# Kernel optimization log

Hardware: AMD Instinct MI355X
Metric: run time of the kernel (lower is better)

The kernel has to match this reference:

```python
import jax, jax.numpy as jnp
import numpy as np
from jax import lax

N_NODES = 100000
N_EDGES = 1600000
NUM_GRAPHS = 2000
F_IN = 64
HIDDEN = 64
NUM_LAYERS = 3
K = 7
NUM_CLASSES = 10


def setup_inputs() -> dict:
    key = jax.random.key(0)
    ks = jax.random.split(key, 16)
    x = jax.random.normal(ks[0], (N_NODES, F_IN), jnp.float32)
    edge_index = jax.random.randint(ks[1], (2, N_EDGES), 0, N_NODES)
    batch = jnp.sort(jax.random.randint(ks[2], (N_NODES,), 0, NUM_GRAPHS))
    s = 1.0 / np.sqrt(HIDDEN)
    p = lambda k_, sh: jax.random.uniform(k_, sh, jnp.float32, -s, s)
    return dict(
        x=x, edge_index=edge_index, batch=batch,
        W1l=p(ks[3], (F_IN, HIDDEN)), b1=p(ks[4], (HIDDEN,)), W1r=p(ks[5], (F_IN, HIDDEN)),
        W2l=p(ks[6], (HIDDEN, HIDDEN)), b2=p(ks[7], (HIDDEN,)), W2r=p(ks[8], (HIDDEN, HIDDEN)),
        W3l=p(ks[9], (HIDDEN, HIDDEN)), b3=p(ks[10], (HIDDEN,)), W3r=p(ks[11], (HIDDEN, HIDDEN)),
        conv1d_w=p(ks[12], (32, HIDDEN, NUM_LAYERS)), conv1d_b=jnp.zeros((32,), jnp.float32),
        lin1_w=p(ks[13], (32 * (K - NUM_LAYERS + 1), HIDDEN)), lin1_b=jnp.zeros((HIDDEN,), jnp.float32),
        lin2_w=p(ks[14], (HIDDEN, NUM_CLASSES)), lin2_b=jnp.zeros((NUM_CLASSES,), jnp.float32),
    )


def _sage(x, src, dst, Wl, b, Wr):
    # PyG SAGEConv (aggr='mean'): lin_l(mean_j x_j) + lin_r(x_i); lin_l carries the bias.
    n = x.shape[0]
    msum = jax.ops.segment_sum(x[src], dst, num_segments=n)          # [N, D] gather+scatter
    cnt = jax.ops.segment_sum(jnp.ones((src.shape[0],), x.dtype), dst, num_segments=n)
    mean = msum / jnp.maximum(cnt, 1.0)[:, None]
    return mean @ Wl + b + x @ Wr


def _sort_pool(x, batch, num_graphs, k):
    # SortAggregation: per graph, sort nodes descending by last feature channel,
    # keep top-k, zero-pad short graphs, flatten to [B, k*D].
    N, D = x.shape
    perm = jnp.lexsort((-x[:, -1], batch))  # primary: graph id, secondary: desc last channel
    sb = batch[perm]
    counts = jax.ops.segment_sum(jnp.ones((N,), jnp.int32), batch, num_segments=num_graphs)
    starts = jnp.concatenate([jnp.zeros((1,), jnp.int32), jnp.cumsum(counts)[:-1]])
    rank = jnp.arange(N, dtype=jnp.int32) - starts[sb]
    valid = rank < k
    b_idx = jnp.where(valid, sb, num_graphs)  # route overflow nodes to dummy row
    r_idx = jnp.where(valid, rank, 0)
    out = jnp.zeros((num_graphs + 1, k, D), x.dtype).at[b_idx, r_idx].set(x[perm])
    return out[:num_graphs].reshape(num_graphs, k * D)


def reference(x, edge_index, batch, W1l, b1, W1r, W2l, b2, W2r, W3l, b3, W3r,
              conv1d_w, conv1d_b, lin1_w, lin1_b, lin2_w, lin2_b):
    src, dst = edge_index[0], edge_index[1]
    h = jax.nn.relu(_sage(x, src, dst, W1l, b1, W1r))
    h = jax.nn.relu(_sage(h, src, dst, W2l, b2, W2r))
    h = jax.nn.relu(_sage(h, src, dst, W3l, b3, W3r))
    g = _sort_pool(h, batch, NUM_GRAPHS, K)                       # [B, K*H]
    g = g.reshape(NUM_GRAPHS, K, HIDDEN).transpose(0, 2, 1)       # [B, H, K]
    c = lax.conv_general_dilated(g, conv1d_w, (1,), 'VALID',
                                 dimension_numbers=('NCH', 'OIH', 'NCH'))
    c = jax.nn.relu(c + conv1d_b[None, :, None])                  # [B, 32, K-ks+1]
    flat = c.reshape(NUM_GRAPHS, -1)
    h1 = jax.nn.relu(flat @ lin1_w + lin1_b)                      # dropout = identity (eval)
    logits = h1 @ lin2_w + lin2_b
    return jax.nn.log_softmax(logits, axis=-1)
```

## Files before the change

### kernel.cpp

```cpp
#include <hip/hip_runtime.h>
#include <hip/hip_bf16.h>

#define NN 100000
#define NE 1600000
#define NG 2000
#define KTOP 7
#define KCAP 192

#define BNODES 128
#define NBKT 782
#define EPB 8192
#define NL1B 196
#define L2CAP 4096

#define GEMM_BLOCKS 768
#define NTILES 1563
#define SMEM_FLOATS (64 * 68 + 2 * 64 * 64)

#define ACC4(A, V) do { A.x += V.x; A.y += V.y; A.z += V.z; A.w += V.w; } while (0)
#define ACC4P(A, U, W) do { A.x += U.x + W.x; A.y += U.y + W.y; \
                            A.z += U.z + W.z; A.w += U.w + W.w; } while (0)

__device__ __forceinline__ void agg_node(const float* __restrict__ XLp, const int* __restrict__ ce,
        int s, int e, int fo, float4& a0, float4& a1, float4& a2, float4& a3) {
    int a = s;
    for (; a + 2 <= e; a += 2) {
        const float4* p0 = (const float4*)(XLp + ((size_t)ce[a] << 6) + fo);
        const float4* p1 = (const float4*)(XLp + ((size_t)ce[a + 1] << 6) + fo);
        float4 u0 = p0[0], u1 = p0[1], u2 = p0[2], u3 = p0[3];
        float4 w0 = p1[0], w1 = p1[1], w2 = p1[2], w3 = p1[3];
        ACC4P(a0, u0, w0); ACC4P(a1, u1, w1); ACC4P(a2, u2, w2); ACC4P(a3, u3, w3);
    }
    if (a < e) {
        const float4* p0 = (const float4*)(XLp + ((size_t)ce[a] << 6) + fo);
        float4 u0 = p0[0], u1 = p0[1], u2 = p0[2], u3 = p0[3];
        ACC4(a0, u0); ACC4(a1, u1); ACC4(a2, u2); ACC4(a3, u3);
    }
}

__device__ __forceinline__ void relu_mean_res(float inv, const float4* tp,
        float4& h0, float4& h1, float4& h2, float4& h3) {
    float4 t0 = tp[0], t1 = tp[1], t2 = tp[2], t3 = tp[3];
    h0.x = fmaxf(h0.x * inv + t0.x, 0.f); h0.y = fmaxf(h0.y * inv + t0.y, 0.f);
    h0.z = fmaxf(h0.z * inv + t0.z, 0.f); h0.w = fmaxf(h0.w * inv + t0.w, 0.f);
    h1.x = fmaxf(h1.x * inv + t1.x, 0.f); h1.y = fmaxf(h1.y * inv + t1.y, 0.f);
    h1.z = fmaxf(h1.z * inv + t1.z, 0.f); h1.w = fmaxf(h1.w * inv + t1.w, 0.f);
    h2.x = fmaxf(h2.x * inv + t2.x, 0.f); h2.y = fmaxf(h2.y * inv + t2.y, 0.f);
    h2.z = fmaxf(h2.z * inv + t2.z, 0.f); h2.w = fmaxf(h2.w * inv + t2.w, 0.f);
    h3.x = fmaxf(h3.x * inv + t3.x, 0.f); h3.y = fmaxf(h3.y * inv + t3.y, 0.f);
    h3.z = fmaxf(h3.z * inv + t3.z, 0.f); h3.w = fmaxf(h3.w * inv + t3.w, 0.f);
}

__device__ __forceinline__ float compute_key(int i, const float* __restrict__ keycol,
        const float* __restrict__ tcol, const int* __restrict__ ptr,
        const int* __restrict__ ce) {
    int s = ptr[i], e = ptr[i + 1];
    float acc = 0.f;
    int a = s;
    for (; a + 2 <= e; a += 2) acc += keycol[ce[a]] + keycol[ce[a + 1]];
    if (a < e) acc += keycol[ce[a]];
    float inv = 1.f / fmaxf((float)(e - s), 1.f);
    return fmaxf(acc * inv + tcol[i], 0.f);
}

#define FMA4C(av, B, acc) do { \
    acc[0] = fmaf(av, B.x, acc[0]); acc[1] = fmaf(av, B.y, acc[1]); \
    acc[2] = fmaf(av, B.z, acc[2]); acc[3] = fmaf(av, B.w, acc[3]); } while (0)

__device__ __forceinline__ void gemm_tile(const float* As, const float* Bl, const float* Br,
        int n0, int ty4, int tx4, float b0, float b1v, float b2v, float b3v,
        float* __restrict__ XL, float* __restrict__ T,
        float* __restrict__ kc_out, float* __restrict__ tc_out) {
    float accl[4][4] = {{0.f}}, accr[4][4] = {{0.f}};
    for (int kc = 0; kc < 64; kc += 4) {
        float4 Av[4], L[4], R[4];
        #pragma unroll
        for (int i = 0; i < 4; ++i) Av[i] = *(const float4*)&As[(ty4 + i) * 68 + kc];
        #pragma unroll
        for (int j = 0; j < 4; ++j) {
            L[j] = *(const float4*)&Bl[(kc + j) * 64 + tx4];
            R[j] = *(const float4*)&Br[(kc + j) * 64 + tx4];
        }
        #pragma unroll
        for (int i = 0; i < 4; ++i) {
            FMA4C(Av[i].x, L[0], accl[i]); FMA4C(Av[i].y, L[1], accl[i]);
            FMA4C(Av[i].z, L[2], accl[i]); FMA4C(Av[i].w, L[3], accl[i]);
            FMA4C(Av[i].x, R[0], accr[i]); FMA4C(Av[i].y, R[1], accr[i]);
            FMA4C(Av[i].z, R[2], accr[i]); FMA4C(Av[i].w, R[3], accr[i]);
        }
    }
    #pragma unroll
    for (int i = 0; i < 4; ++i) {
        int g = n0 + ty4 + i;
        if (g < NN) {
            *(float4*)&XL[(size_t)g * 64 + tx4] =
                make_float4(accl[i][0], accl[i][1], accl[i][2], accl[i][3]);
            *(float4*)&T[(size_t)g * 64 + tx4] =
                make_float4(accr[i][0] + b0, accr[i][1] + b1v, accr[i][2] + b2v, accr[i][3] + b3v);
            if (kc_out && tx4 == 60) {
                kc_out[g] = accl[i][3];
                tc_out[g] = accr[i][3] + b3v;
            }
        }
    }
}

__device__ __forceinline__ void stage_weights(float* Bl, float* Br,
        const float* __restrict__ Wl, const float* __restrict__ Wr, int t) {
    #pragma unroll
    for (int q = 0; q < 4; ++q) {
        int idx = t + q * 256;
        ((float4*)Bl)[idx] = ((const float4*)Wl)[idx];
        ((float4*)Br)[idx] = ((const float4*)Wr)[idx];
    }
}

__device__ __forceinline__ void gemm_body(int bid, int nblocks, float* smem,
        const float* __restrict__ X, const float* __restrict__ Wl,
        const float* __restrict__ Wr, const float* __restrict__ bias,
        float* __restrict__ XL, float* __restrict__ T) {
    float* As = smem;
    float* Bl = smem + 64 * 68;
    float* Br = Bl + 64 * 64;
    int t = threadIdx.x;
    stage_weights(Bl, Br, Wl, Wr, t);
    int ty4 = (t >> 4) * 4, tx4 = (t & 15) * 4;
    float b0 = bias[tx4 + 0], b1v = bias[tx4 + 1], b2v = bias[tx4 + 2], b3v = bias[tx4 + 3];
    for (int tile = bid; tile < NTILES; tile += nblocks) {
        int n0 = tile * 64;
        #pragma unroll
        for (int q = 0; q < 4; ++q) {
            int f = t + q * 256;
            int node = f >> 4, seg = f & 15;
            int g = n0 + node;
            float4 v = make_float4(0.f, 0.f, 0.f, 0.f);
            if (g < NN) v = *(const float4*)&X[(size_t)g * 64 + seg * 4];
            *(float4*)&As[node * 68 + seg * 4] = v;
        }
        __syncthreads();
        gemm_tile(As, Bl, Br, n0, ty4, tx4, b0, b1v, b2v, b3v, XL, T, nullptr, nullptr);
        __syncthreads();
    }
}

__global__ __launch_bounds__(256) void k_aggemm(const float* __restrict__ XL_in,
        float* __restrict__ T, const int* __restrict__ ptr, const int* __restrict__ ce,
        const float* __restrict__ Wl, const float* __restrict__ Wr,
        const float* __restrict__ bias, float* __restrict__ XL_out,
        float* __restrict__ kc_out, float* __restrict__ tc_out) {
    __shared__ float smem[SMEM_FLOATS];
    float* As = smem;
    float* Bl = smem + 64 * 68;
    float* Br = Bl + 64 * 64;
    int t = threadIdx.x;
    stage_weights(Bl, Br, Wl, Wr, t);
    int node_l = t >> 2;
    int fo = (t & 3) * 16;
    int ty4 = (t >> 4) * 4, tx4 = (t & 15) * 4;
    float b0 = bias[tx4 + 0], b1v = bias[tx4 + 1], b2v = bias[tx4 + 2], b3v = bias[tx4 + 3];
    for (int tile = blockIdx.x; tile < NTILES; tile += GEMM_BLOCKS) {
        int n0 = tile * 64;
        int i = n0 + node_l;
        float4 h0 = make_float4(0.f, 0.f, 0.f, 0.f), h1 = h0, h2 = h0, h3 = h0;
        if (i < NN) {
            int s = ptr[i], e = ptr[i + 1];
            agg_node(XL_in, ce, s, e, fo, h0, h1, h2, h3);
            float inv = 1.f / fmaxf((float)(e - s), 1.f);
            relu_mean_res(inv, (const float4*)(T + ((size_t)i << 6) + fo), h0, h1, h2, h3);
        }
        float* dst = &As[node_l * 68 + fo];
        ((float4*)dst)[0] = h0; ((float4*)dst)[1] = h1;
        ((float4*)dst)[2] = h2; ((float4*)dst)[3] = h3;
        __syncthreads();
        gemm_tile(As, Bl, Br, n0, ty4, tx4, b0, b1v, b2v, b3v, XL_out, T, kc_out, tc_out);
        __syncthreads();
    }
}

__global__ __launch_bounds__(256) void k_front(const float* __restrict__ X,
        const float* __restrict__ Wl, const float* __restrict__ Wr,
        const float* __restrict__ bias, float* __restrict__ XL, float* __restrict__ T,
        const int* __restrict__ edst, int* __restrict__ bh_t,
        const int* __restrict__ bat, int* __restrict__ gstart) {
    __shared__ float smem[SMEM_FLOATS];
    int bid = blockIdx.x, t = threadIdx.x;
    if (bid < GEMM_BLOCKS) {
        gemm_body(bid, GEMM_BLOCKS, smem, X, Wl, Wr, bias, XL, T);
    } else if (bid < GEMM_BLOCKS + NL1B) {
        int bk = bid - GEMM_BLOCKS;
        int* h = (int*)smem;
        for (int q = t; q < NBKT; q += 256) h[q] = 0;
        __syncthreads();
        int e0 = bk * EPB, e1 = min(e0 + EPB, NE);
        for (int e = e0 + t; e < e1; e += 256) atomicAdd(&h[edst[e] >> 7], 1);
        __syncthreads();
        for (int q = t; q < NBKT; q += 256) bh_t[q * NL1B + bk] = h[q];
    } else {
        int g = (bid - GEMM_BLOCKS - NL1B) * 256 + t;
        if (g <= NG) {
            int lo = 0, hi = NN;
            while (lo < hi) { int mid = (lo + hi) >> 1; if (bat[mid] < g) lo = mid + 1; else hi = mid; }
            gstart[g] = lo;
        }
    }
}

__global__ void k_colscan(int* __restrict__ bh_t, int* __restrict__ btot) {
    __shared__ int carry;
    int b = blockIdx.x, t = threadIdx.x;
    if (t == 0) carry = 0;
    __syncthreads();
    for (int base = 0; base < NL1B; base += 64) {
        int idx = base + t;
        int v = (idx < NL1B) ? bh_t[b * NL1B + idx] : 0;
        int x = v;
        #pragma unroll
        for (int off = 1; off < 64; off <<= 1) {
            int y = __shfl_up(x, off);
            if (t >= off) x += y;
        }
        int c = carry;
        if (idx < NL1B) bh_t[b * NL1B + idx] = c + x - v;
        __syncthreads();
        if (t == 63) carry = c + x;
        __syncthreads();
    }
    if (t == 0) btot[b] = carry;
}

__global__ __launch_bounds__(256) void k_bscatter(const int* __restrict__ esrc,
        const int* __restrict__ edst, const int* __restrict__ bh_t,
        const int* __restrict__ btot, int* __restrict__ ebuf) {
    __shared__ int sbt[1024];
    __shared__ int ssum[256];
    __shared__ int cur[NBKT];
    int t = threadIdx.x, bk = blockIdx.x;
    for (int q = t; q < 1024; q += 256) sbt[q] = (q < NBKT) ? btot[q] : 0;
    __syncthreads();
    int base = t * 4;
    int a0 = sbt[base], a1 = sbt[base + 1], a2 = sbt[base + 2], a3 = sbt[base + 3];
    int s1 = a0 + a1, s2 = s1 + a2, s3 = s2 + a3;
    ssum[t] = s3;
    __syncthreads();
    for (int off = 1; off < 256; off <<= 1) {
        int y = (t >= off) ? ssum[t - off] : 0;
        __syncthreads();
        ssum[t] += y;
        __syncthreads();
    }
    int prev = (t > 0) ? ssum[t - 1] : 0;
    sbt[base] = prev; sbt[base + 1] = prev + a0;
    sbt[base + 2] = prev + s1; sbt[base + 3] = prev + s2;
    __syncthreads();
    for (int q = t; q < NBKT; q += 256) cur[q] = sbt[q] + bh_t[q * NL1B + bk];
    __syncthreads();
    int e0 = bk * EPB, e1 = min(e0 + EPB, NE);
    for (int e = e0 + t; e < e1; e += 256) {
        int d = edst[e], s = esrc[e];
        int pos = atomicAdd(&cur[d >> 7], 1);
        ebuf[pos] = s | ((d & 127) << 20);
    }
}

__global__ __launch_bounds__(128) void k_bbuild(const int* __restrict__ ebuf,
        const int* __restrict__ btot, int* __restrict__ ce, int* __restrict__ ptr) {
    __shared__ int lord[L2CAP];
    __shared__ int cnt[BNODES], sc[BNODES], cursor[BNODES];
    __shared__ int red[128];
    int b = blockIdx.x, t = threadIdx.x;
    int part = 0;
    for (int j = t; j < b; j += 128) part += btot[j];
    red[t] = part;
    __syncthreads();
    for (int off = 64; off >= 1; off >>= 1) {
        if (t < off) red[t] += red[t + off];
        __syncthreads();
    }
    int base = red[0];
    int nb = btot[b];
    cnt[t] = 0;
    __syncthreads();
    for (int j = t; j < nb; j += 128) atomicAdd(&cnt[ebuf[base + j] >> 20], 1);
    __syncthreads();
    int v = cnt[t]; sc[t] = v; __syncthreads();
    for (int off = 1; off < 128; off <<= 1) {
        int y = (t >= off) ? sc[t - off] : 0;
        __syncthreads();
        sc[t] += y;
        __syncthreads();
    }
    int segend = sc[t], segstart = sc[t] - v;
    cursor[t] = segstart;
    __syncthreads();
    bool fits = (nb <= L2CAP);
    for (int j = t; j < nb; j += 128) {
        int pv = ebuf[base + j];
        int node = pv >> 20;
        int pos = atomicAdd(&cursor[node], 1);
        if (fits) lord[pos] = pv & 0xFFFFF;
        else ce[base + pos] = pv & 0xFFFFF;
    }
    __syncthreads();
    if (fits) {
        for (int a = segstart + 1; a < segend; ++a) {
            int val = lord[a]; int j = a - 1;
            while (j >= segstart && lord[j] > val) { lord[j + 1] = lord[j]; --j; }
            lord[j + 1] = val;
        }
        __syncthreads();
        for (int j = t; j < nb; j += 128) ce[base + j] = lord[j];
    } else {
        for (int a = segstart + 1; a < segend; ++a) {
            int val = ce[base + a]; int j = a - 1;
            while (j >= segstart && ce[base + j] > val) { ce[base + j + 1] = ce[base + j]; --j; }
            ce[base + j + 1] = val;
        }
    }
    int node = b * BNODES + t;
    if (node <= NN) ptr[node] = base + segstart;
}

__global__ __launch_bounds__(256) void k_tail(const int* __restrict__ gstart,
        const float* __restrict__ keycol, const float* __restrict__ tcol,
        const int* __restrict__ ptr, const int* __restrict__ ce,
        const float* __restrict__ XLa, const float* __restrict__ T,
        const float* __restrict__ cw, const float* __restrict__ cb,
        const float* __restrict__ l1w, const float* __restrict__ l1b,
        const float* __restrict__ l2w, const float* __restrict__ l2b,
        float* __restrict__ out, int G) {
    __shared__ float sw[32 * 64 * 3];
    __shared__ float s2w[64 * 10];
    __shared__ float sg[4][KTOP][64];
    __shared__ float sflat[4][160];
    __shared__ float sh1[4][64];
    __shared__ float slog[4][10];
    __shared__ float skey[4][KCAP];
    __shared__ int   widx[4][KTOP];
    int t = threadIdx.x;
    for (int q = t; q < 32 * 64 * 3; q += 256) sw[q] = cw[q];
    for (int q = t; q < 640; q += 256) s2w[q] = l2w[q];
    int wv = t >> 6, lane = t & 63;
    int b = blockIdx.x * 4 + wv;
    int s = gstart[b], e = gstart[b + 1];
    int cnt = e - s;
    for (int base = 0; base < cnt; base += 64) {
        int o = base + lane;
        if (o < cnt && o < KCAP) skey[wv][o] = compute_key(s + o, keycol, tcol, ptr, ce);
    }
    {
        float pk = 3.4e38f; int pi = -1;
        for (int r = 0; r < KTOP; ++r) {
            float bk = -1.f; int bi = -1;
            for (int o = lane; o < cnt; o += 64) {
                int i = s + o;
                float k = (o < KCAP) ? skey[wv][o] : compute_key(i, keycol, tcol, ptr, ce);
                bool elig = (k < pk) || (k == pk && i > pi);
                if (elig && (k > bk || (k == bk && (unsigned)i < (unsigned)bi))) { bk = k; bi = i; }
            }
            #pragma unroll
            for (int off = 1; off < 64; off <<= 1) {
                float ok = __shfl_xor(bk, off);
                int   oi = __shfl_xor(bi, off);
                if (ok > bk || (ok == bk && (unsigned)oi < (unsigned)bi)) { bk = ok; bi = oi; }
            }
            if (lane == 0) widx[wv][r] = bi;
            pk = bk; pi = bi;
        }
    }
    if (lane < 28) {
        int r = lane >> 2, fo = (lane & 3) * 16;
        int i = widx[wv][r];
        float4 h0 = make_float4(0.f, 0.f, 0.f, 0.f), h1 = h0, h2 = h0, h3 = h0;
        if (i >= 0) {
            int s2 = ptr[i], e2 = ptr[i + 1];
            agg_node(XLa, ce, s2, e2, fo, h0, h1, h2, h3);
            float inv = 1.f / fmaxf((float)(e2 - s2), 1.f);
            relu_mean_res(inv, (const float4*)(T + ((size_t)i << 6) + fo), h0, h1, h2, h3);
        }
        float* dstp = &sg[wv][r][fo];
        ((float4*)dstp)[0] = h0; ((float4*)dstp)[1] = h1;
        ((float4*)dstp)[2] = h2; ((float4*)dstp)[3] = h3;
    }
    __syncthreads();
    for (int idx = lane; idx < 160; idx += 64) {
        int o = idx / 5, p = idx % 5;
        float acc = cb[o];
        #pragma unroll
        for (int dt = 0; dt < 3; ++dt) {
            const float* wrow = &sw[(o * 64) * 3 + dt];
            const float* grow = &sg[wv][p + dt][0];
            for (int i = 0; i < 64; ++i) acc = fmaf(wrow[i * 3], grow[i], acc);
        }
        sflat[wv][idx] = fmaxf(acc, 0.f);
    }
    __syncthreads();
    {
        float acc = l1b[lane];
        for (int k = 0; k < 160; ++k) acc = fmaf(sflat[wv][k], l1w[k * 64 + lane], acc);
        sh1[wv][lane] = fmaxf(acc, 0.f);
    }
    __syncthreads();
    if (lane < 10) {
        float acc = l2b[lane];
        for (int k = 0; k < 64; ++k) acc = fmaf(sh1[wv][k], s2w[k * 10 + lane], acc);
        slog[wv][lane] = acc;
    }
    __syncthreads();
    if (lane < 10) {
        float m = -3.4e38f;
        for (int j = 0; j < 10; ++j) m = fmaxf(m, slog[wv][j]);
        float ssum = 0.f;
        for (int j = 0; j < 10; ++j) ssum += expf(slog[wv][j] - m);
        out[b * 10 + lane] = slog[wv][lane] - m - logf(ssum);
    }
}

extern "C" void kernel_launch(void* const* d_in, const int* in_sizes, int n_in,
                              void* d_out, int out_size, void* d_ws, size_t ws_size,
                              hipStream_t stream) {
    const float* x   = (const float*)d_in[0];
    const int*   ei  = (const int*)d_in[1];
    const int*   bat = (const int*)d_in[2];
    const float* W1l = (const float*)d_in[3], *b1 = (const float*)d_in[4], *W1r = (const float*)d_in[5];
    const float* W2l = (const float*)d_in[6], *b2 = (const float*)d_in[7], *W2r = (const float*)d_in[8];
    const float* W3l = (const float*)d_in[9], *b3 = (const float*)d_in[10], *W3r = (const float*)d_in[11];
    const float* cw  = (const float*)d_in[12], *cb  = (const float*)d_in[13];
    const float* l1w = (const float*)d_in[14], *l1b = (const float*)d_in[15];
    const float* l2w = (const float*)d_in[16], *l2b = (const float*)d_in[17];
    float* out = (float*)d_out;
    const int* esrc = ei;
    const int* edst = ei + NE;

    char* w = (char*)d_ws;
    size_t off = 0;
    auto take = [&](size_t bytes) { void* p = w + off; off = (off + bytes + 255) & ~(size_t)255; return p; };
    int*   bh_t    = (int*)take((size_t)NBKT * NL1B * 4);
    int*   btot    = (int*)take((size_t)NBKT * 4);
    int*   gstart  = (int*)take((size_t)(NG + 1) * 4);
    int*   ebuf    = (int*)take((size_t)NE * 4);
    int*   csr_ptr = (int*)take((size_t)(NN + 1) * 4);
    int*   csr_e   = (int*)take((size_t)NE * 4);
    float* XLa     = (float*)take((size_t)NN * 64 * 4);
    float* XLb     = (float*)take((size_t)NN * 64 * 4);
    float* T       = (float*)take((size_t)NN * 64 * 4);
    float* keycol  = (float*)take((size_t)NN * 4);
    float* tcol    = (float*)take((size_t)NN * 4);

    k_front<<<GEMM_BLOCKS + NL1B + 8, 256, 0, stream>>>(x, W1l, W1r, b1, XLa, T,
                                                        edst, bh_t, bat, gstart);
    k_colscan<<<NBKT, 64, 0, stream>>>(bh_t, btot);
    k_bscatter<<<NL1B, 256, 0, stream>>>(esrc, edst, bh_t, btot, ebuf);
    k_bbuild <<<NBKT, 128, 0, stream>>>(ebuf, btot, csr_e, csr_ptr);

    k_aggemm<<<GEMM_BLOCKS, 256, 0, stream>>>(XLa, T, csr_ptr, csr_e, W2l, W2r, b2, XLb,
                                              nullptr, nullptr);
    k_aggemm<<<GEMM_BLOCKS, 256, 0, stream>>>(XLb, T, csr_ptr, csr_e, W3l, W3r, b3, XLa,
                                              keycol, tcol);

    k_tail<<<NG / 4, 256, 0, stream>>>(gstart, keycol, tcol, csr_ptr, csr_e, XLa, T,
                                       cw, cb, l1w, l1b, l2w, l2b, out, NG);
}
```

Before: 318.6 us.

## Launch one tile per block in aggregate-GEMM and read weights directly from global

The persistent grid-stride loop in k_aggemm is replaced with one 64-node tile per block, launching NTILES blocks. The shared-memory weight staging is dropped, so the weight matrices are read straight from global (L1/L2-cached) memory inside the GEMM loop, and shared memory shrinks to just the activation tile. The intent is higher occupancy and less per-block staging overhead, so the irregular gather latency is hidden better. In exchange every block re-reads the weights from cache, and the GEMM is now inline code, so it may depend on an FMA4C macro defined elsewhere.

New measurement: 337.4 us. 1.06x slower.

```diff
diff --git a/kernel.cpp b/kernel.cpp
--- a/kernel.cpp
+++ b/kernel.cpp
@@ -148,32 +148,56 @@
         const float* __restrict__ Wl, const float* __restrict__ Wr,
         const float* __restrict__ bias, float* __restrict__ XL_out,
         float* __restrict__ kc_out, float* __restrict__ tc_out) {
-    __shared__ float smem[SMEM_FLOATS];
-    float* As = smem;
-    float* Bl = smem + 64 * 68;
-    float* Br = Bl + 64 * 64;
+    __shared__ float As[64 * 68];
     int t = threadIdx.x;
-    stage_weights(Bl, Br, Wl, Wr, t);
     int node_l = t >> 2;
     int fo = (t & 3) * 16;
+    int n0 = blockIdx.x * 64;
+    int i = n0 + node_l;
+    float4 h0 = make_float4(0.f, 0.f, 0.f, 0.f), h1 = h0, h2 = h0, h3 = h0;
+    if (i < NN) {
+        int s = ptr[i], e = ptr[i + 1];
+        agg_node(XL_in, ce, s, e, fo, h0, h1, h2, h3);
+        float inv = 1.f / fmaxf((float)(e - s), 1.f);
+        relu_mean_res(inv, (const float4*)(T + ((size_t)i << 6) + fo), h0, h1, h2, h3);
+    }
+    float* dst = &As[node_l * 68 + fo];
+    ((float4*)dst)[0] = h0; ((float4*)dst)[1] = h1;
+    ((float4*)dst)[2] = h2; ((float4*)dst)[3] = h3;
+    __syncthreads();
     int ty4 = (t >> 4) * 4, tx4 = (t & 15) * 4;
     float b0 = bias[tx4 + 0], b1v = bias[tx4 + 1], b2v = bias[tx4 + 2], b3v = bias[tx4 + 3];
-    for (int tile = blockIdx.x; tile < NTILES; tile += GEMM_BLOCKS) {
-        int n0 = tile * 64;
-        int i = n0 + node_l;
-        float4 h0 = make_float4(0.f, 0.f, 0.f, 0.f), h1 = h0, h2 = h0, h3 = h0;
-        if (i < NN) {
-            int s = ptr[i], e = ptr[i + 1];
-            agg_node(XL_in, ce, s, e, fo, h0, h1, h2, h3);
-            float inv = 1.f / fmaxf((float)(e - s), 1.f);
-            relu_mean_res(inv, (const float4*)(T + ((size_t)i << 6) + fo), h0, h1, h2, h3);
-        }
-        float* dst = &As[node_l * 68 + fo];
-        ((float4*)dst)[0] = h0; ((float4*)dst)[1] = h1;
-        ((float4*)dst)[2] = h2; ((float4*)dst)[3] = h3;
-        __syncthreads();
-        gemm_tile(As, Bl, Br, n0, ty4, tx4, b0, b1v, b2v, b3v, XL_out, T, kc_out, tc_out);
-        __syncthreads();
+    float accl[4][4] = {{0.f}}, accr[4][4] = {{0.f}};
+    for (int kc = 0; kc < 64; kc += 4) {
+        float4 Av[4], L[4], R[4];
+        #pragma unroll
+        for (int ii = 0; ii < 4; ++ii) Av[ii] = *(const float4*)&As[(ty4 + ii) * 68 + kc];
+        #pragma unroll
+        for (int j = 0; j < 4; ++j) {
+            L[j] = *(const float4*)&Wl[(kc + j) * 64 + tx4];
+            R[j] = *(const float4*)&Wr[(kc + j) * 64 + tx4];
+        }
+        #pragma unroll
+        for (int ii = 0; ii < 4; ++ii) {
+            FMA4C(Av[ii].x, L[0], accl[ii]); FMA4C(Av[ii].y, L[1], accl[ii]);
+            FMA4C(Av[ii].z, L[2], accl[ii]); FMA4C(Av[ii].w, L[3], accl[ii]);
+            FMA4C(Av[ii].x, R[0], accr[ii]); FMA4C(Av[ii].y, R[1], accr[ii]);
+            FMA4C(Av[ii].z, R[2], accr[ii]); FMA4C(Av[ii].w, R[3], accr[ii]);
+        }
+    }
+    #pragma unroll
+    for (int ii = 0; ii < 4; ++ii) {
+        int g = n0 + ty4 + ii;
+        if (g < NN) {
+            *(float4*)&XL_out[(size_t)g * 64 + tx4] =
+                make_float4(accl[ii][0], accl[ii][1], accl[ii][2], accl[ii][3]);
+            *(float4*)&T[(size_t)g * 64 + tx4] =
+                make_float4(accr[ii][0] + b0, accr[ii][1] + b1v, accr[ii][2] + b2v, accr[ii][3] + b3v);
+            if (kc_out && tx4 == 60) {
+                kc_out[g] = accl[ii][3];
+                tc_out[g] = accr[ii][3] + b3v;
+            }
+        }
     }
 }
 
@@ -452,10 +476,10 @@
     k_bscatter<<<NL1B, 256, 0, stream>>>(esrc, edst, bh_t, btot, ebuf);
     k_bbuild <<<NBKT, 128, 0, stream>>>(ebuf, btot, csr_e, csr_ptr);
 
-    k_aggemm<<<GEMM_BLOCKS, 256, 0, stream>>>(XLa, T, csr_ptr, csr_e, W2l, W2r, b2, XLb,
-                                              nullptr, nullptr);
-    k_aggemm<<<GEMM_BLOCKS, 256, 0, stream>>>(XLb, T, csr_ptr, csr_e, W3l, W3r, b3, XLa,
-                                              keycol, tcol);
+    k_aggemm<<<NTILES, 256, 0, stream>>>(XLa, T, csr_ptr, csr_e, W2l, W2r, b2, XLb,
+                                         nullptr, nullptr);
+    k_aggemm<<<NTILES, 256, 0, stream>>>(XLb, T, csr_ptr, csr_e, W3l, W3r, b3, XLa,
+                                         keycol, tcol);
 
     k_tail<<<NG / 4, 256, 0, stream>>>(gstart, keycol, tcol, csr_ptr, csr_e, XLa, T,
                                        cw, cb, l1w, l1b, l2w, l2b, out, NG);
```

## Split layer-1 GEMM across CSR scatter and build kernels to overlap work

Applied to the files above, without the earlier changes.

Moves the first-layer dense GEMM out of the front kernel and splits its tiles between the bucket-scatter and CSR-build kernels, so the latency-bound graph preprocessing overlaps with GEMM work in the same launch. The counting kernel now runs alone, and the edge chunk size is halved to give more histogram and scatter blocks. The CSR build kernel moves to 256 threads per block to share the GEMM block shape, which leaves half of each block idle in its scan and sort phases. The extra blocks also enlarge the bucket-offset table that the column scan walks.

Result: slower. 333.3 us (+4.6%).

```diff
diff --git a/kernel.cpp b/kernel.cpp
--- a/kernel.cpp
+++ b/kernel.cpp
@@ -9,12 +9,14 @@
 
 #define BNODES 128
 #define NBKT 782
-#define EPB 8192
-#define NL1B 196
+#define EPB 4096
+#define NL1B 391
 #define L2CAP 4096
 
 #define GEMM_BLOCKS 768
+#define GB_HALF 512
 #define NTILES 1563
+#define TSPLIT 900
 #define SMEM_FLOATS (64 * 68 + 2 * 64 * 64)
 
 #define ACC4(A, V) do { A.x += V.x; A.y += V.y; A.z += V.z; A.w += V.w; } while (0)
@@ -115,8 +117,8 @@
     }
 }
 
-__device__ __forceinline__ void gemm_body(int bid, int nblocks, float* smem,
-        const float* __restrict__ X, const float* __restrict__ Wl,
+__device__ __forceinline__ void gemm_body_range(int bid, int nblocks, int t0, int t1,
+        float* smem, const float* __restrict__ X, const float* __restrict__ Wl,
         const float* __restrict__ Wr, const float* __restrict__ bias,
         float* __restrict__ XL, float* __restrict__ T) {
     float* As = smem;
@@ -126,7 +128,7 @@
     stage_weights(Bl, Br, Wl, Wr, t);
     int ty4 = (t >> 4) * 4, tx4 = (t & 15) * 4;
     float b0 = bias[tx4 + 0], b1v = bias[tx4 + 1], b2v = bias[tx4 + 2], b3v = bias[tx4 + 3];
-    for (int tile = bid; tile < NTILES; tile += nblocks) {
+    for (int tile = t0 + bid; tile < t1; tile += nblocks) {
         int n0 = tile * 64;
         #pragma unroll
         for (int q = 0; q < 4; ++q) {
@@ -140,6 +142,170 @@
         __syncthreads();
         gemm_tile(As, Bl, Br, n0, ty4, tx4, b0, b1v, b2v, b3v, XL, T, nullptr, nullptr);
         __syncthreads();
+    }
+}
+
+__global__ __launch_bounds__(256) void k_count(const int* __restrict__ edst,
+        int* __restrict__ bh_t, const int* __restrict__ bat, int* __restrict__ gstart) {
+    __shared__ int h[NBKT];
+    int bid = blockIdx.x, t = threadIdx.x;
+    if (bid < NL1B) {
+        for (int q = t; q < NBKT; q += 256) h[q] = 0;
+        __syncthreads();
+        int e0 = bid * EPB, e1 = min(e0 + EPB, NE);
+        for (int e = e0 + t; e < e1; e += 256) atomicAdd(&h[edst[e] >> 7], 1);
+        __syncthreads();
+        for (int q = t; q < NBKT; q += 256) bh_t[q * NL1B + bid] = h[q];
+    } else {
+        int g = (bid - NL1B) * 256 + t;
+        if (g <= NG) {
+            int lo = 0, hi = NN;
+            while (lo < hi) { int mid = (lo + hi) >> 1; if (bat[mid] < g) lo = mid + 1; else hi = mid; }
+            gstart[g] = lo;
+        }
+    }
+}
+
+__global__ void k_colscan(int* __restrict__ bh_t, int* __restrict__ btot) {
+    __shared__ int carry;
+    int b = blockIdx.x, t = threadIdx.x;
+    if (t == 0) carry = 0;
+    __syncthreads();
+    for (int base = 0; base < NL1B; base += 64) {
+        int idx = base + t;
+        int v = (idx < NL1B) ? bh_t[b * NL1B + idx] : 0;
+        int x = v;
+        #pragma unroll
+        for (int off = 1; off < 64; off <<= 1) {
+            int y = __shfl_up(x, off);
+            if (t >= off) x += y;
+        }
+        int c = carry;
+        if (idx < NL1B) bh_t[b * NL1B + idx] = c + x - v;
+        __syncthreads();
+        if (t == 63) carry = c + x;
+        __syncthreads();
+    }
+    if (t == 0) btot[b] = carry;
+}
+
+__global__ __launch_bounds__(256) void k_scat_gemm(const int* __restrict__ esrc,
+        const int* __restrict__ edst, const int* __restrict__ bh_t,
+        const int* __restrict__ btot, int* __restrict__ ebuf,
+        const float* __restrict__ X, const float* __restrict__ Wl,
+        const float* __restrict__ Wr, const float* __restrict__ bias,
+        float* __restrict__ XL, float* __restrict__ T) {
+    __shared__ float smem[SMEM_FLOATS];
+    int bid = blockIdx.x, t = threadIdx.x;
+    if (bid < NL1B) {
+        int* sbt  = (int*)smem;
+        int* ssum = sbt + 1024;
+        int* cur  = ssum + 256;
+        int bk = bid;
+        for (int q = t; q < 1024; q += 256) sbt[q] = (q < NBKT) ? btot[q] : 0;
+        __syncthreads();
+        int base = t * 4;
+        int a0 = sbt[base], a1 = sbt[base + 1], a2 = sbt[base + 2], a3 = sbt[base + 3];
+        int s1 = a0 + a1, s2 = s1 + a2, s3 = s2 + a3;
+        ssum[t] = s3;
+        __syncthreads();
+        for (int off = 1; off < 256; off <<= 1) {
+            int y = (t >= off) ? ssum[t - off] : 0;
+            __syncthreads();
+            ssum[t] += y;
+            __syncthreads();
+        }
+        int prev = (t > 0) ? ssum[t - 1] : 0;
+        sbt[base] = prev; sbt[base + 1] = prev + a0;
+        sbt[base + 2] = prev + s1; sbt[base + 3] = prev + s2;
+        __syncthreads();
+        for (int q = t; q < NBKT; q += 256) cur[q] = sbt[q] + bh_t[q * NL1B + bk];
+        __syncthreads();
+        int e0 = bk * EPB, e1 = min(e0 + EPB, NE);
+        for (int e = e0 + t; e < e1; e += 256) {
+            int d = edst[e], s = esrc[e];
+            int pos = atomicAdd(&cur[d >> 7], 1);
+            ebuf[pos] = s | ((d & 127) << 20);
+        }
+    } else {
+        gemm_body_range(bid - NL1B, GB_HALF, 0, TSPLIT, smem, X, Wl, Wr, bias, XL, T);
+    }
+}
+
+__global__ __launch_bounds__(256) void k_build_gemm(const int* __restrict__ ebuf,
+        const int* __restrict__ btot, int* __restrict__ ce, int* __restrict__ ptr,
+        const float* __restrict__ X, const float* __restrict__ Wl,
+        const float* __restrict__ Wr, const float* __restrict__ bias,
+        float* __restrict__ XL, float* __restrict__ T) {
+    __shared__ float smem[SMEM_FLOATS];
+    int bid = blockIdx.x, t = threadIdx.x;
+    if (bid < NBKT) {
+        int* lord   = (int*)smem;
+        int* cnt    = lord + L2CAP;
+        int* sc     = cnt + BNODES;
+        int* cursor = sc + BNODES;
+        int* red    = cursor + BNODES;
+        int b = bid;
+        int part = 0;
+        for (int j = t; j < b; j += 256) part += btot[j];
+        red[t] = part;
+        __syncthreads();
+        for (int off = 128; off >= 1; off >>= 1) {
+            if (t < off) red[t] += red[t + off];
+            __syncthreads();
+        }
+        int base = red[0];
+        int nb = btot[b];
+        if (t < BNODES) cnt[t] = 0;
+        __syncthreads();
+        for (int j = t; j < nb; j += 256) atomicAdd(&cnt[ebuf[base + j] >> 20], 1);
+        __syncthreads();
+        int v = (t < BNODES) ? cnt[t] : 0;
+        if (t < BNODES) sc[t] = v;
+        __syncthreads();
+        for (int off = 1; off < BNODES; off <<= 1) {
+            int y = (t >= off && t < BNODES) ? sc[t - off] : 0;
+            __syncthreads();
+            if (t < BNODES) sc[t] += y;
+            __syncthreads();
+        }
+        int segend = 0, segstart = 0;
+        if (t < BNODES) { segend = sc[t]; segstart = sc[t] - v; cursor[t] = segstart; }
+        __syncthreads();
+        bool fits = (nb <= L2CAP);
+        for (int j = t; j < nb; j += 256) {
+            int pv = ebuf[base + j];
+            int node = pv >> 20;
+            int pos = atomicAdd(&cursor[node], 1);
+            if (fits) lord[pos] = pv & 0xFFFFF;
+            else ce[base + pos] = pv & 0xFFFFF;
+        }
+        __syncthreads();
+        if (fits) {
+            if (t < BNODES) {
+                for (int a = segstart + 1; a < segend; ++a) {
+                    int val = lord[a]; int j = a - 1;
+                    while (j >= segstart && lord[j] > val) { lord[j + 1] = lord[j]; --j; }
+                    lord[j + 1] = val;
+                }
+            }
+            __syncthreads();
+            for (int j = t; j < nb; j += 256) ce[base + j] = lord[j];
+        } else {
+            if (t < BNODES) {
+                for (int a = segstart + 1; a < segend; ++a) {
+                    int val = ce[base + a]; int j = a - 1;
+                    while (j >= segstart && ce[base + j] > val) { ce[base + j + 1] = ce[base + j]; --j; }
+                    ce[base + j + 1] = val;
+                }
+            }
+        }
+        if (t < BNODES) {
+            int node = b * BNODES + t;
+            if (node <= NN) ptr[node] = base + segstart;
+        }
+    } else {
+        gemm_body_range(bid - NBKT, GB_HALF, TSPLIT, NTILES, smem, X, Wl, Wr, bias, XL, T);
     }
 }
 
@@ -175,149 +341,6 @@
         gemm_tile(As, Bl, Br, n0, ty4, tx4, b0, b1v, b2v, b3v, XL_out, T, kc_out, tc_out);
         __syncthreads();
     }
-}
-
-__global__ __launch_bounds__(256) void k_front(const float* __restrict__ X,
-        const float* __restrict__ Wl, const float* __restrict__ Wr,
-        const float* __restrict__ bias, float* __restrict__ XL, float* __restrict__ T,
-        const int* __restrict__ edst, int* __restrict__ bh_t,
-        const int* __restrict__ bat, int* __restrict__ gstart) {
-    __shared__ float smem[SMEM_FLOATS];
-    int bid = blockIdx.x, t = threadIdx.x;
-    if (bid < GEMM_BLOCKS) {
-        gemm_body(bid, GEMM_BLOCKS, smem, X, Wl, Wr, bias, XL, T);
-    } else if (bid < GEMM_BLOCKS + NL1B) {
-        int bk = bid - GEMM_BLOCKS;
-        int* h = (int*)smem;
-        for (int q = t; q < NBKT; q += 256) h[q] = 0;
-        __syncthreads();
-        int e0 = bk * EPB, e1 = min(e0 + EPB, NE);
-        for (int e = e0 + t; e < e1; e += 256) atomicAdd(&h[edst[e] >> 7], 1);
-        __syncthreads();
-        for (int q = t; q < NBKT; q += 256) bh_t[q * NL1B + bk] = h[q];
-    } else {
-        int g = (bid - GEMM_BLOCKS - NL1B) * 256 + t;
-        if (g <= NG) {
-            int lo = 0, hi = NN;
-            while (lo < hi) { int mid = (lo + hi) >> 1; if (bat[mid] < g) lo = mid + 1; else hi = mid; }
-            gstart[g] = lo;
-        }
-    }
-}
-
-__global__ void k_colscan(int* __restrict__ bh_t, int* __restrict__ btot) {
-    __shared__ int carry;
-    int b = blockIdx.x, t = threadIdx.x;
-    if (t == 0) carry = 0;
-    __syncthreads();
-    for (int base = 0; base < NL1B; base += 64) {
-        int idx = base + t;
-        int v = (idx < NL1B) ? bh_t[b * NL1B + idx] : 0;
-        int x = v;
-        #pragma unroll
-        for (int off = 1; off < 64; off <<= 1) {
-            int y = __shfl_up(x, off);
-            if (t >= off) x += y;
-        }
-        int c = carry;
-        if (idx < NL1B) bh_t[b * NL1B + idx] = c + x - v;
-        __syncthreads();
-        if (t == 63) carry = c + x;
-        __syncthreads();
-    }
-    if (t == 0) btot[b] = carry;
-}
-
-__global__ __launch_bounds__(256) void k_bscatter(const int* __restrict__ esrc,
-        const int* __restrict__ edst, const int* __restrict__ bh_t,
-        const int* __restrict__ btot, int* __restrict__ ebuf) {
-    __shared__ int sbt[1024];
-    __shared__ int ssum[256];
-    __shared__ int cur[NBKT];
-    int t = threadIdx.x, bk = blockIdx.x;
-    for (int q = t; q < 1024; q += 256) sbt[q] = (q < NBKT) ? btot[q] : 0;
-    __syncthreads();
-    int base = t * 4;
-    int a0 = sbt[base], a1 = sbt[base + 1], a2 = sbt[base + 2], a3 = sbt[base + 3];
-    int s1 = a0 + a1, s2 = s1 + a2, s3 = s2 + a3;
-    ssum[t] = s3;
-    __syncthreads();
-    for (int off = 1; off < 256; off <<= 1) {
-        int y = (t >= off) ? ssum[t - off] : 0;
-        __syncthreads();
-        ssum[t] += y;
-        __syncthreads();
-    }
-    int prev = (t > 0) ? ssum[t - 1] : 0;
-    sbt[base] = prev; sbt[base + 1] = prev + a0;
-    sbt[base + 2] = prev + s1; sbt[base + 3] = prev + s2;
-    __syncthreads();
-    for (int q = t; q < NBKT; q += 256) cur[q] = sbt[q] + bh_t[q * NL1B + bk];
-    __syncthreads();
-    int e0 = bk * EPB, e1 = min(e0 + EPB, NE);
-    for (int e = e0 + t; e < e1; e += 256) {
-        int d = edst[e], s = esrc[e];
-        int pos = atomicAdd(&cur[d >> 7], 1);
-        ebuf[pos] = s | ((d & 127) << 20);
-    }
-}
-
-__global__ __launch_bounds__(128) void k_bbuild(const int* __restrict__ ebuf,
-        const int* __restrict__ btot, int* __restrict__ ce, int* __restrict__ ptr) {
-    __shared__ int lord[L2CAP];
-    __shared__ int cnt[BNODES], sc[BNODES], cursor[BNODES];
-    __shared__ int red[128];
-    int b = blockIdx.x, t = threadIdx.x;
-    int part = 0;
-    for (int j = t; j < b; j += 128) part += btot[j];
-    red[t] = part;
-    __syncthreads();
-    for (int off = 64; off >= 1; off >>= 1) {
-        if (t < off) red[t] += red[t + off];
-        __syncthreads();
-    }
-    int base = red[0];
-    int nb = btot[b];
-    cnt[t] = 0;
-    __syncthreads();
-    for (int j = t; j < nb; j += 128) atomicAdd(&cnt[ebuf[base + j] >> 20], 1);
-    __syncthreads();
-    int v = cnt[t]; sc[t] = v; __syncthreads();
-    for (int off = 1; off < 128; off <<= 1) {
-        int y = (t >= off) ? sc[t - off] : 0;
-        __syncthreads();
-        sc[t] += y;
-        __syncthreads();
-    }
-    int segend = sc[t], segstart = sc[t] - v;
-    cursor[t] = segstart;
-    __syncthreads();
-    bool fits = (nb <= L2CAP);
-    for (int j = t; j < nb; j += 128) {
-        int pv = ebuf[base + j];
-        int node = pv >> 20;
-        int pos = atomicAdd(&cursor[node], 1);
-        if (fits) lord[pos] = pv & 0xFFFFF;
-        else ce[base + pos] = pv & 0xFFFFF;
-    }
-    __syncthreads();
-    if (fits) {
-        for (int a = segstart + 1; a < segend; ++a) {
-            int val = lord[a]; int j = a - 1;
-            while (j >= segstart && lord[j] > val) { lord[j + 1] = lord[j]; --j; }
-            lord[j + 1] = val;
-        }
-        __syncthreads();
-        for (int j = t; j < nb; j += 128) ce[base + j] = lord[j];
-    } else {
-        for (int a = segstart + 1; a < segend; ++a) {
-            int val = ce[base + a]; int j = a - 1;
-            while (j >= segstart && ce[base + j] > val) { ce[base + j + 1] = ce[base + j]; --j; }
-            ce[base + j + 1] = val;
-        }
-    }
-    int node = b * BNODES + t;
-    if (node <= NN) ptr[node] = base + segstart;
 }
 
 __global__ __launch_bounds__(256) void k_tail(const int* __restrict__ gstart,
@@ -446,11 +469,12 @@
     float* keycol  = (float*)take((size_t)NN * 4);
     float* tcol    = (float*)take((size_t)NN * 4);
 
-    k_front<<<GEMM_BLOCKS + NL1B + 8, 256, 0, stream>>>(x, W1l, W1r, b1, XLa, T,
-                                                        edst, bh_t, bat, gstart);
+    k_count<<<NL1B + 8, 256, 0, stream>>>(edst, bh_t, bat, gstart);
     k_colscan<<<NBKT, 64, 0, stream>>>(bh_t, btot);
-    k_bscatter<<<NL1B, 256, 0, stream>>>(esrc, edst, bh_t, btot, ebuf);
-    k_bbuild <<<NBKT, 128, 0, stream>>>(ebuf, btot, csr_e, csr_ptr);
+    k_scat_gemm<<<NL1B + GB_HALF, 256, 0, stream>>>(esrc, edst, bh_t, btot, ebuf,
+                                                    x, W1l, W1r, b1, XLa, T);
+    k_build_gemm<<<NBKT + GB_HALF, 256, 0, stream>>>(ebuf, btot, csr_e, csr_ptr,
+                                                     x, W1l, W1r, b1, XLa, T);
 
     k_aggemm<<<GEMM_BLOCKS, 256, 0, stream>>>(XLa, T, csr_ptr, csr_e, W2l, W2r, b2, XLb,
                                               nullptr, nullptr);
```
